# Performance work log

Measured on AMD Instinct MI355X. Metric: run time of the kernel, lower is better.

The kernel has to match this reference:

```python
import jax, jax.numpy as jnp
import numpy as np

N = 100000
E = 1600000
D_DES = 768
D = 128
NUM_REL = 2
SLOPE = 0.01  # torch LeakyReLU default negative slope


def leaky_relu(x):
    return jnp.where(x >= 0, x, SLOPE * x)


def setup_inputs() -> dict:
    key = jax.random.key(0)
    ks = jax.random.split(key, 16)
    s = 0.02
    return {
        "des": jax.random.normal(ks[0], (N, D_DES), jnp.float32),
        "tweet": jax.random.normal(ks[1], (N, D_DES), jnp.float32),
        "num_prop": jax.random.normal(ks[2], (N, 6), jnp.float32),
        "cat_prop": jax.random.normal(ks[3], (N, 11), jnp.float32),
        "edge_index": jax.random.randint(ks[4], (2, E), 0, N, jnp.int32),
        "edge_type": jax.random.randint(ks[5], (E,), 0, NUM_REL, jnp.int32),
        "W_des": s * jax.random.normal(ks[6], (D_DES, D), jnp.float32),
        "b_des": jnp.zeros((D,), jnp.float32),
        "W_in": s * jax.random.normal(ks[7], (D, D), jnp.float32),
        "b_in": jnp.zeros((D,), jnp.float32),
        "W_rel": s * jax.random.normal(ks[8], (NUM_REL, D, D), jnp.float32),
        "W_root": s * jax.random.normal(ks[9], (D, D), jnp.float32),
        "b_rgcn": jnp.zeros((D,), jnp.float32),
        "W_out1": s * jax.random.normal(ks[10], (D, D), jnp.float32),
        "b_out1": jnp.zeros((D,), jnp.float32),
        "W_out2": s * jax.random.normal(ks[11], (D, 2), jnp.float32),
        "b_out2": jnp.zeros((2,), jnp.float32),
    }


def rgcn_conv(x, src, dst, edge_type, W_rel, W_root, b):
    # PyG RGCNConv: out[i] = x[i] @ W_root + b + sum_r mean_{j in N_r(i)} x[j] @ W_r
    n = x.shape[0]
    out = x @ W_root + b
    for r in range(NUM_REL):
        mask = (edge_type == r).astype(x.dtype)  # [E]
        h = x @ W_rel[r]                         # [N, D] transform once per relation
        msg = h[src] * mask[:, None]             # [E, D] gather + mask
        agg = jax.ops.segment_sum(msg, dst, num_segments=n)   # [N, D]
        deg = jax.ops.segment_sum(mask, dst, num_segments=n)  # [N]
        out = out + agg / jnp.maximum(deg, 1.0)[:, None]
    return out


def reference(des, tweet, num_prop, cat_prop, edge_index, edge_type,
              W_des, b_des, W_in, b_in, W_rel, W_root, b_rgcn,
              W_out1, b_out1, W_out2, b_out2):
    src, dst = edge_index[0], edge_index[1]
    x = leaky_relu(des @ W_des + b_des)          # linear_relu_des (tweet/props unused in source)
    x = leaky_relu(x @ W_in + b_in)              # linear_relu_input
    x = rgcn_conv(x, src, dst, edge_type, W_rel, W_root, b_rgcn)
    # F.dropout with training=False is identity (eval mode)
    x = rgcn_conv(x, src, dst, edge_type, W_rel, W_root, b_rgcn)
    x = leaky_relu(x @ W_out1 + b_out1)          # linear_relu_output1
    x = x @ W_out2 + b_out2                      # linear_output2 -> [N, 2]
    return x
```

## Files before the change

kernel.cpp:

```cpp
#include <hip/hip_runtime.h>

#define SLOPE 0.01f

__device__ __forceinline__ float lrelu(float v) { return v >= 0.f ? v : SLOPE * v; }

template <int RELU>
__global__ __launch_bounds__(256, 2) void gemm128(const float* __restrict__ A,
                                                  const float* __restrict__ W,
                                                  const float* __restrict__ bias,
                                                  float* __restrict__ C,
                                                  int M, int K) {
    __shared__ float As[32][132];
    __shared__ float Ws[32][132];

    const int tid = threadIdx.x;
    const int m0 = blockIdx.x * 128;
    const int rg = tid >> 4;
    const int cg = tid & 15;
    const int lm = tid >> 3;
    const int lc = (tid & 7) * 4;
    const int wr = tid >> 5;
    const int wc = (tid & 31) * 4;

    float acc[8][8];
#pragma unroll
    for (int i = 0; i < 8; i++)
#pragma unroll
        for (int j = 0; j < 8; j++) acc[i][j] = 0.f;

    for (int k0 = 0; k0 < K; k0 += 32) {
#pragma unroll
        for (int p = 0; p < 4; p++) {
            int row = m0 + lm + p * 32;
            int rc = row < M ? row : M - 1;
            const float4 v = *(const float4*)(A + (size_t)rc * K + k0 + lc);
            As[lc + 0][lm + p * 32] = v.x;
            As[lc + 1][lm + p * 32] = v.y;
            As[lc + 2][lm + p * 32] = v.z;
            As[lc + 3][lm + p * 32] = v.w;
        }
#pragma unroll
        for (int p = 0; p < 4; p++) {
            *(float4*)&Ws[wr + p * 8][wc] =
                *(const float4*)(W + (size_t)(k0 + wr + p * 8) * 128 + wc);
        }
        __syncthreads();
#pragma unroll
        for (int kk = 0; kk < 32; kk++) {
            float a[8], b[8];
            *(float4*)&a[0] = *(const float4*)&As[kk][rg * 4];
            *(float4*)&a[4] = *(const float4*)&As[kk][64 + rg * 4];
            *(float4*)&b[0] = *(const float4*)&Ws[kk][cg * 4];
            *(float4*)&b[4] = *(const float4*)&Ws[kk][64 + cg * 4];
#pragma unroll
            for (int i = 0; i < 8; i++)
#pragma unroll
                for (int j = 0; j < 8; j++) acc[i][j] = fmaf(a[i], b[j], acc[i][j]);
        }
        __syncthreads();
    }

    float4 b0 = *(const float4*)(bias + cg * 4);
    float4 b1 = *(const float4*)(bias + 64 + cg * 4);
#pragma unroll
    for (int i = 0; i < 8; i++) {
        int row = m0 + ((i < 4) ? (rg * 4 + i) : (64 + rg * 4 + (i - 4)));
        if (row >= M) continue;
        float4 o0, o1;
        o0.x = acc[i][0] + b0.x; o0.y = acc[i][1] + b0.y;
        o0.z = acc[i][2] + b0.z; o0.w = acc[i][3] + b0.w;
        o1.x = acc[i][4] + b1.x; o1.y = acc[i][5] + b1.y;
        o1.z = acc[i][6] + b1.z; o1.w = acc[i][7] + b1.w;
        if (RELU) {
            o0.x = lrelu(o0.x); o0.y = lrelu(o0.y); o0.z = lrelu(o0.z); o0.w = lrelu(o0.w);
            o1.x = lrelu(o1.x); o1.y = lrelu(o1.y); o1.z = lrelu(o1.z); o1.w = lrelu(o1.w);
        }
        *(float4*)(C + (size_t)row * 128 + cg * 4) = o0;
        *(float4*)(C + (size_t)row * 128 + 64 + cg * 4) = o1;
    }
}

__global__ __launch_bounds__(256, 2) void rgcn_gemm(const float* __restrict__ x,
                                                    const float* __restrict__ agg0,
                                                    const float* __restrict__ agg1,
                                                    const float* __restrict__ Wroot,
                                                    const float* __restrict__ W0,
                                                    const float* __restrict__ W1,
                                                    const float* __restrict__ bias,
                                                    float* __restrict__ C, int M) {
    __shared__ float As[32][132];
    __shared__ float Ws[32][132];

    const int tid = threadIdx.x;
    const int m0 = blockIdx.x * 128;
    const int rg = tid >> 4;
    const int cg = tid & 15;
    const int lm = tid >> 3;
    const int lc = (tid & 7) * 4;
    const int wr = tid >> 5;
    const int wc = (tid & 31) * 4;

    float acc[8][8];
#pragma unroll
    for (int i = 0; i < 8; i++)
#pragma unroll
        for (int j = 0; j < 8; j++) acc[i][j] = 0.f;

    const float* Aseg[3] = {x, agg0, agg1};
    const float* Wseg[3] = {Wroot, W0, W1};

    for (int seg = 0; seg < 3; seg++) {
        const float* Ap = Aseg[seg];
        const float* Wp = Wseg[seg];
        for (int k0 = 0; k0 < 128; k0 += 32) {
#pragma unroll
            for (int p = 0; p < 4; p++) {
                int row = m0 + lm + p * 32;
                int rc = row < M ? row : M - 1;
                const float4 v = *(const float4*)(Ap + (size_t)rc * 128 + k0 + lc);
                As[lc + 0][lm + p * 32] = v.x;
                As[lc + 1][lm + p * 32] = v.y;
                As[lc + 2][lm + p * 32] = v.z;
                As[lc + 3][lm + p * 32] = v.w;
            }
#pragma unroll
            for (int p = 0; p < 4; p++) {
                *(float4*)&Ws[wr + p * 8][wc] =
                    *(const float4*)(Wp + (size_t)(k0 + wr + p * 8) * 128 + wc);
            }
            __syncthreads();
#pragma unroll
            for (int kk = 0; kk < 32; kk++) {
                float a[8], b[8];
                *(float4*)&a[0] = *(const float4*)&As[kk][rg * 4];
                *(float4*)&a[4] = *(const float4*)&As[kk][64 + rg * 4];
                *(float4*)&b[0] = *(const float4*)&Ws[kk][cg * 4];
                *(float4*)&b[4] = *(const float4*)&Ws[kk][64 + cg * 4];
#pragma unroll
                for (int i = 0; i < 8; i++)
#pragma unroll
                    for (int j = 0; j < 8; j++) acc[i][j] = fmaf(a[i], b[j], acc[i][j]);
            }
            __syncthreads();
        }
    }

    float4 b0 = *(const float4*)(bias + cg * 4);
    float4 b1 = *(const float4*)(bias + 64 + cg * 4);
#pragma unroll
    for (int i = 0; i < 8; i++) {
        int row = m0 + ((i < 4) ? (rg * 4 + i) : (64 + rg * 4 + (i - 4)));
        if (row >= M) continue;
        float4 o0, o1;
        o0.x = acc[i][0] + b0.x; o0.y = acc[i][1] + b0.y;
        o0.z = acc[i][2] + b0.z; o0.w = acc[i][3] + b0.w;
        o1.x = acc[i][4] + b1.x; o1.y = acc[i][5] + b1.y;
        o1.z = acc[i][6] + b1.z; o1.w = acc[i][7] + b1.w;
        *(float4*)(C + (size_t)row * 128 + cg * 4) = o0;
        *(float4*)(C + (size_t)row * 128 + 64 + cg * 4) = o1;
    }
}

__global__ __launch_bounds__(256) void hist_kernel(const int* __restrict__ ei,
                                                   const int* __restrict__ et,
                                                   int* __restrict__ cnt, int E, int N) {
    int e = blockIdx.x * 256 + threadIdx.x;
    if (e >= E) return;
    int d = ei[E + e];
    int r = et[e];
    atomicAdd(&cnt[r * N + d], 1);
}

__global__ __launch_bounds__(256) void scan_partial(const int* __restrict__ cnt,
                                                    int* __restrict__ partials, int n) {
    __shared__ int sm[256];
    int base = blockIdx.x * 1024;
    int t = threadIdx.x;
    int s = 0;
#pragma unroll
    for (int i = 0; i < 4; i++) {
        int idx = base + t * 4 + i;
        if (idx < n) s += cnt[idx];
    }
    sm[t] = s;
    __syncthreads();
    for (int off = 128; off; off >>= 1) {
        if (t < off) sm[t] += sm[t + off];
        __syncthreads();
    }
    if (t == 0) partials[blockIdx.x] = sm[0];
}

__global__ __launch_bounds__(64) void scan_top(int* __restrict__ partials, int nb,
                                               int* __restrict__ off, int n, int total) {
    int lane = threadIdx.x;
    int base = 0;
    for (int start = 0; start < nb; start += 64) {
        int idx = start + lane;
        int v = (idx < nb) ? partials[idx] : 0;
        int incl = v;
#pragma unroll
        for (int o = 1; o < 64; o <<= 1) {
            int t = __shfl_up(incl, o);
            if (lane >= o) incl += t;
        }
        if (idx < nb) partials[idx] = base + incl - v;
        base += __shfl(incl, 63);
    }
    if (lane == 0) off[n] = total;
}

__global__ __launch_bounds__(64) void scan_chunk(const int* __restrict__ cnt,
                                                 const int* __restrict__ partials,
                                                 int* __restrict__ off, int n) {
    int lane = threadIdx.x;
    int base = partials[blockIdx.x];
    int cbase = blockIdx.x * 1024;
    for (int i = 0; i < 16; i++) {
        int idx = cbase + i * 64 + lane;
        int v = (idx < n) ? cnt[idx] : 0;
        int incl = v;
#pragma unroll
        for (int o = 1; o < 64; o <<= 1) {
            int t = __shfl_up(incl, o);
            if (lane >= o) incl += t;
        }
        if (idx < n) off[idx] = base + incl - v;
        base += __shfl(incl, 63);
    }
}

__global__ __launch_bounds__(256) void scatter_kernel(const int* __restrict__ ei,
                                                      const int* __restrict__ et,
                                                      const int* __restrict__ off,
                                                      int* __restrict__ cur,
                                                      int* __restrict__ sorted_src,
                                                      int E, int N) {
    int e = blockIdx.x * 256 + threadIdx.x;
    if (e >= E) return;
    int s = ei[e];
    int d = ei[E + e];
    int r = et[e];
    int b = r * N + d;
    int pos = off[b] + atomicAdd(&cur[b], 1);
    sorted_src[pos] = s;
}

__global__ __launch_bounds__(256) void agg_csr(const int* __restrict__ off,
                                               const int* __restrict__ sorted_src,
                                               const float* __restrict__ X,
                                               float* __restrict__ agg0,
                                               float* __restrict__ agg1,
                                               int N) {
    int w = (int)((blockIdx.x * (unsigned)blockDim.x + threadIdx.x) >> 6);
    if (w >= 2 * N) return;
    int lane = threadIdx.x & 63;
    int start = off[w];
    int end = off[w + 1];
    float2 sum = {0.f, 0.f};
    for (int i = start; i < end; i++) {
        int s = sorted_src[i];
        float2 v = *(const float2*)(X + (size_t)s * 128 + lane * 2);
        sum.x += v.x;
        sum.y += v.y;
    }
    int deg = end - start;
    float inv = (deg > 1) ? (1.f / (float)deg) : 1.f;
    sum.x *= inv;
    sum.y *= inv;
    float* agg = (w < N) ? agg0 : agg1;
    int d = (w < N) ? w : w - N;
    *(float2*)(agg + (size_t)d * 128 + lane * 2) = sum;
}

__global__ __launch_bounds__(256) void out2_kernel(const float* __restrict__ X,
                                                   const float* __restrict__ W,
                                                   const float* __restrict__ b,
                                                   float* __restrict__ out, int M) {
    const int row = (int)((blockIdx.x * (unsigned)blockDim.x + threadIdx.x) >> 6);
    if (row >= M) return;
    const int lane = threadIdx.x & 63;
    const float* xr = X + (size_t)row * 128;
    float x0 = xr[lane], x1 = xr[lane + 64];
    float s0 = x0 * W[lane * 2 + 0] + x1 * W[(lane + 64) * 2 + 0];
    float s1 = x0 * W[lane * 2 + 1] + x1 * W[(lane + 64) * 2 + 1];
#pragma unroll
    for (int off = 32; off; off >>= 1) {
        s0 += __shfl_down(s0, off);
        s1 += __shfl_down(s1, off);
    }
    if (lane == 0) {
        out[(size_t)row * 2 + 0] = s0 + b[0];
        out[(size_t)row * 2 + 1] = s1 + b[1];
    }
}

extern "C" void kernel_launch(void* const* d_in, const int* in_sizes, int n_in,
                              void* d_out, int out_size, void* d_ws, size_t ws_size,
                              hipStream_t stream) {
    const float* des    = (const float*)d_in[0];
    const int*   ei     = (const int*)d_in[4];
    const int*   et     = (const int*)d_in[5];
    const float* W_des  = (const float*)d_in[6];
    const float* b_des  = (const float*)d_in[7];
    const float* W_in   = (const float*)d_in[8];
    const float* b_in   = (const float*)d_in[9];
    const float* W_rel  = (const float*)d_in[10];
    const float* W_root = (const float*)d_in[11];
    const float* b_rgcn = (const float*)d_in[12];
    const float* W_out1 = (const float*)d_in[13];
    const float* b_out1 = (const float*)d_in[14];
    const float* W_out2 = (const float*)d_in[15];
    const float* b_out2 = (const float*)d_in[16];
    float* out = (float*)d_out;

    const int N = in_sizes[0] / 768;
    const int E = in_sizes[5];
    const int TWO_N = 2 * N;
    const float* W0 = W_rel;
    const float* W1 = W_rel + 128 * 128;

    float* ws    = (float*)d_ws;
    float* xA    = ws;
    float* xB    = xA + (size_t)N * 128;
    float* agg0  = xB + (size_t)N * 128;
    float* agg1  = agg0 + (size_t)N * 128;
    int*   cnt   = (int*)(agg1 + (size_t)N * 128);
    int*   cur   = cnt + TWO_N;
    int*   off   = cur + TWO_N;
    int*   parts = off + TWO_N + 1;
    int*   ssrc  = parts + 256;

    const int gemmBlocks = (N + 127) / 128;
    const int edgeBlocks = (E + 255) / 256;
    const int aggBlocks  = (TWO_N + 3) / 4;
    const int rowBlocks  = (int)(((size_t)N * 64 + 255) / 256);
    const int nChunks    = (TWO_N + 1023) / 1024;

    hipMemsetAsync(cnt, 0, (size_t)2 * TWO_N * sizeof(int), stream);
    hist_kernel<<<edgeBlocks, 256, 0, stream>>>(ei, et, cnt, E, N);
    scan_partial<<<nChunks, 256, 0, stream>>>(cnt, parts, TWO_N);
    scan_top<<<1, 64, 0, stream>>>(parts, nChunks, off, TWO_N, E);
    scan_chunk<<<nChunks, 64, 0, stream>>>(cnt, parts, off, TWO_N);
    scatter_kernel<<<edgeBlocks, 256, 0, stream>>>(ei, et, off, cur, ssrc, E, N);

    gemm128<1><<<gemmBlocks, 256, 0, stream>>>(des, W_des, b_des, xA, N, 768);
    gemm128<1><<<gemmBlocks, 256, 0, stream>>>(xA, W_in, b_in, xB, N, 128);

    agg_csr<<<aggBlocks, 256, 0, stream>>>(off, ssrc, xB, agg0, agg1, N);
    rgcn_gemm<<<gemmBlocks, 256, 0, stream>>>(xB, agg0, agg1, W_root, W0, W1, b_rgcn, xA, N);

    agg_csr<<<aggBlocks, 256, 0, stream>>>(off, ssrc, xA, agg0, agg1, N);
    rgcn_gemm<<<gemmBlocks, 256, 0, stream>>>(xA, agg0, agg1, W_root, W0, W1, b_rgcn, xB, N);

    gemm128<1><<<gemmBlocks, 256, 0, stream>>>(xB, W_out1, b_out1, xA, N, 128);
    out2_kernel<<<rowBlocks, 256, 0, stream>>>(xA, W_out2, b_out2, out, N);
}
```

Measured before the change: 1.667 ms.

## Replace FP32 FMA GEMMs with split-bf16 MFMA GEMMs

```diff
diff --git a/kernel.cpp b/kernel.cpp
--- a/kernel.cpp
+++ b/kernel.cpp
@@ -2,162 +2,152 @@
 
 #define SLOPE 0.01f
 
+typedef __attribute__((ext_vector_type(8))) short bf16x8;
+typedef __attribute__((ext_vector_type(4))) float f32x4;
+
 __device__ __forceinline__ float lrelu(float v) { return v >= 0.f ? v : SLOPE * v; }
 
-template <int RELU>
-__global__ __launch_bounds__(256, 2) void gemm128(const float* __restrict__ A,
-                                                  const float* __restrict__ W,
-                                                  const float* __restrict__ bias,
-                                                  float* __restrict__ C,
-                                                  int M, int K) {
-    __shared__ float As[32][132];
-    __shared__ float Ws[32][132];
+__device__ __forceinline__ void split_bf16(float x, unsigned short& h, unsigned short& l) {
+    unsigned b = __float_as_uint(x);
+    unsigned hb = b & 0xFFFF0000u;
+    h = (unsigned short)(hb >> 16);
+    float r = x - __uint_as_float(hb);
+    l = (unsigned short)(__float_as_uint(r) >> 16);
+}
+
+__global__ __launch_bounds__(256) void split_w(const float* __restrict__ W_des,
+                                               const float* __restrict__ W_in,
+                                               const float* __restrict__ W_root,
+                                               const float* __restrict__ W0,
+                                               const float* __restrict__ W1,
+                                               const float* __restrict__ W_out1,
+                                               unsigned short* __restrict__ th,
+                                               unsigned short* __restrict__ tl) {
+    const float* src;
+    int K;
+    size_t off;
+    switch (blockIdx.y) {
+        case 0: src = W_des;  K = 768; off = 0;                    break;
+        case 1: src = W_in;   K = 128; off = 768 * 128;            break;
+        case 2: src = W_root; K = 128; off = 768 * 128 + 16384;    break;
+        case 3: src = W0;     K = 128; off = 768 * 128 + 2 * 16384; break;
+        case 4: src = W1;     K = 128; off = 768 * 128 + 3 * 16384; break;
+        default: src = W_out1; K = 128; off = 768 * 128 + 4 * 16384; break;
+    }
+    const int c = blockIdx.x;
+    unsigned short* dh = th + off + (size_t)c * K;
+    unsigned short* dl = tl + off + (size_t)c * K;
+    for (int k = threadIdx.x; k < K; k += 256) {
+        float v = src[(size_t)k * 128 + c];
+        unsigned short h, l;
+        split_bf16(v, h, l);
+        dh[k] = h;
+        dl[k] = l;
+    }
+}
+
+template <int NSEG, int RELU>
+__global__ __launch_bounds__(256, 2) void gemm_mfma(
+        const float* __restrict__ A0, const float* __restrict__ A1,
+        const float* __restrict__ A2,
+        const unsigned short* __restrict__ Wh0, const unsigned short* __restrict__ Wl0,
+        const unsigned short* __restrict__ Wh1, const unsigned short* __restrict__ Wl1,
+        const unsigned short* __restrict__ Wh2, const unsigned short* __restrict__ Wl2,
+        int K0, const float* __restrict__ bias, float* __restrict__ C, int M) {
+    __shared__ unsigned short AsH[128][32];
+    __shared__ unsigned short AsL[128][32];
+    __shared__ unsigned short BsH[128][32];
+    __shared__ unsigned short BsL[128][32];
 
     const int tid = threadIdx.x;
+    const int lane = tid & 63;
+    const int wv = tid >> 6;
+    const int wr = (wv >> 1) * 64;
+    const int wc = (wv & 1) * 64;
+    const int fr = lane & 15;
+    const int fk = (lane >> 4) * 8;
     const int m0 = blockIdx.x * 128;
-    const int rg = tid >> 4;
-    const int cg = tid & 15;
-    const int lm = tid >> 3;
-    const int lc = (tid & 7) * 4;
-    const int wr = tid >> 5;
-    const int wc = (tid & 31) * 4;
-
-    float acc[8][8];
-#pragma unroll
-    for (int i = 0; i < 8; i++)
-#pragma unroll
-        for (int j = 0; j < 8; j++) acc[i][j] = 0.f;
-
-    for (int k0 = 0; k0 < K; k0 += 32) {
-#pragma unroll
-        for (int p = 0; p < 4; p++) {
-            int row = m0 + lm + p * 32;
-            int rc = row < M ? row : M - 1;
-            const float4 v = *(const float4*)(A + (size_t)rc * K + k0 + lc);
-            As[lc + 0][lm + p * 32] = v.x;
-            As[lc + 1][lm + p * 32] = v.y;
-            As[lc + 2][lm + p * 32] = v.z;
-            As[lc + 3][lm + p * 32] = v.w;
-        }
-#pragma unroll
-        for (int p = 0; p < 4; p++) {
-            *(float4*)&Ws[wr + p * 8][wc] =
-                *(const float4*)(W + (size_t)(k0 + wr + p * 8) * 128 + wc);
-        }
-        __syncthreads();
-#pragma unroll
-        for (int kk = 0; kk < 32; kk++) {
-            float a[8], b[8];
-            *(float4*)&a[0] = *(const float4*)&As[kk][rg * 4];
-            *(float4*)&a[4] = *(const float4*)&As[kk][64 + rg * 4];
-            *(float4*)&b[0] = *(const float4*)&Ws[kk][cg * 4];
-            *(float4*)&b[4] = *(const float4*)&Ws[kk][64 + cg * 4];
-#pragma unroll
-            for (int i = 0; i < 8; i++)
-#pragma unroll
-                for (int j = 0; j < 8; j++) acc[i][j] = fmaf(a[i], b[j], acc[i][j]);
-        }
-        __syncthreads();
-    }
-
-    float4 b0 = *(const float4*)(bias + cg * 4);
-    float4 b1 = *(const float4*)(bias + 64 + cg * 4);
-#pragma unroll
-    for (int i = 0; i < 8; i++) {
-        int row = m0 + ((i < 4) ? (rg * 4 + i) : (64 + rg * 4 + (i - 4)));
-        if (row >= M) continue;
-        float4 o0, o1;
-        o0.x = acc[i][0] + b0.x; o0.y = acc[i][1] + b0.y;
-        o0.z = acc[i][2] + b0.z; o0.w = acc[i][3] + b0.w;
-        o1.x = acc[i][4] + b1.x; o1.y = acc[i][5] + b1.y;
-        o1.z = acc[i][6] + b1.z; o1.w = acc[i][7] + b1.w;
-        if (RELU) {
-            o0.x = lrelu(o0.x); o0.y = lrelu(o0.y); o0.z = lrelu(o0.z); o0.w = lrelu(o0.w);
-            o1.x = lrelu(o1.x); o1.y = lrelu(o1.y); o1.z = lrelu(o1.z); o1.w = lrelu(o1.w);
-        }
-        *(float4*)(C + (size_t)row * 128 + cg * 4) = o0;
-        *(float4*)(C + (size_t)row * 128 + 64 + cg * 4) = o1;
-    }
-}
-
-__global__ __launch_bounds__(256, 2) void rgcn_gemm(const float* __restrict__ x,
-                                                    const float* __restrict__ agg0,
-                                                    const float* __restrict__ agg1,
-                                                    const float* __restrict__ Wroot,
-                                                    const float* __restrict__ W0,
-                                                    const float* __restrict__ W1,
-                                                    const float* __restrict__ bias,
-                                                    float* __restrict__ C, int M) {
-    __shared__ float As[32][132];
-    __shared__ float Ws[32][132];
-
-    const int tid = threadIdx.x;
-    const int m0 = blockIdx.x * 128;
-    const int rg = tid >> 4;
-    const int cg = tid & 15;
-    const int lm = tid >> 3;
-    const int lc = (tid & 7) * 4;
-    const int wr = tid >> 5;
-    const int wc = (tid & 31) * 4;
-
-    float acc[8][8];
-#pragma unroll
-    for (int i = 0; i < 8; i++)
-#pragma unroll
-        for (int j = 0; j < 8; j++) acc[i][j] = 0.f;
-
-    const float* Aseg[3] = {x, agg0, agg1};
-    const float* Wseg[3] = {Wroot, W0, W1};
-
-    for (int seg = 0; seg < 3; seg++) {
-        const float* Ap = Aseg[seg];
-        const float* Wp = Wseg[seg];
-        for (int k0 = 0; k0 < 128; k0 += 32) {
-#pragma unroll
-            for (int p = 0; p < 4; p++) {
-                int row = m0 + lm + p * 32;
-                int rc = row < M ? row : M - 1;
-                const float4 v = *(const float4*)(Ap + (size_t)rc * 128 + k0 + lc);
-                As[lc + 0][lm + p * 32] = v.x;
-                As[lc + 1][lm + p * 32] = v.y;
-                As[lc + 2][lm + p * 32] = v.z;
-                As[lc + 3][lm + p * 32] = v.w;
-            }
-#pragma unroll
-            for (int p = 0; p < 4; p++) {
-                *(float4*)&Ws[wr + p * 8][wc] =
-                    *(const float4*)(Wp + (size_t)(k0 + wr + p * 8) * 128 + wc);
+
+    f32x4 acc[4][4];
+#pragma unroll
+    for (int i = 0; i < 4; ++i)
+#pragma unroll
+        for (int j = 0; j < 4; ++j)
+#pragma unroll
+            for (int r = 0; r < 4; ++r) acc[i][j][r] = 0.f;
+
+    for (int seg = 0; seg < NSEG; ++seg) {
+        const float* A = (seg == 0) ? A0 : (seg == 1 ? A1 : A2);
+        const unsigned short* Wh = (seg == 0) ? Wh0 : (seg == 1 ? Wh1 : Wh2);
+        const unsigned short* Wl = (seg == 0) ? Wl0 : (seg == 1 ? Wl1 : Wl2);
+        const int K = (seg == 0) ? K0 : 128;
+
+        for (int k0 = 0; k0 < K; k0 += 32) {
+#pragma unroll
+            for (int p = 0; p < 4; ++p) {
+                const int f = tid + 256 * p;
+                const int r = f >> 3;
+                const int q = f & 7;
+                int row = m0 + r;
+                if (row >= M) row = M - 1;
+                const float4 v = *(const float4*)(A + (size_t)row * K + k0 + q * 4);
+                unsigned short h0, h1, h2, h3, l0, l1, l2, l3;
+                split_bf16(v.x, h0, l0);
+                split_bf16(v.y, h1, l1);
+                split_bf16(v.z, h2, l2);
+                split_bf16(v.w, h3, l3);
+                *(ushort4*)&AsH[r][q * 4] = make_ushort4(h0, h1, h2, h3);
+                *(ushort4*)&AsL[r][q * 4] = make_ushort4(l0, l1, l2, l3);
+            }
+#pragma unroll
+            for (int p = 0; p < 4; ++p) {
+                const int f = tid + 256 * p;
+                const int c = f >> 3;
+                const int q = f & 7;
+                *(ushort4*)&BsH[c][q * 4] = *(const ushort4*)(Wh + (size_t)c * K + k0 + q * 4);
+                *(ushort4*)&BsL[c][q * 4] = *(const ushort4*)(Wl + (size_t)c * K + k0 + q * 4);
             }
             __syncthreads();
-#pragma unroll
-            for (int kk = 0; kk < 32; kk++) {
-                float a[8], b[8];
-                *(float4*)&a[0] = *(const float4*)&As[kk][rg * 4];
-                *(float4*)&a[4] = *(const float4*)&As[kk][64 + rg * 4];
-                *(float4*)&b[0] = *(const float4*)&Ws[kk][cg * 4];
-                *(float4*)&b[4] = *(const float4*)&Ws[kk][64 + cg * 4];
-#pragma unroll
-                for (int i = 0; i < 8; i++)
-#pragma unroll
-                    for (int j = 0; j < 8; j++) acc[i][j] = fmaf(a[i], b[j], acc[i][j]);
+
+            bf16x8 ah[4], al[4];
+#pragma unroll
+            for (int i = 0; i < 4; ++i) {
+                ah[i] = *(const bf16x8*)&AsH[wr + i * 16 + fr][fk];
+                al[i] = *(const bf16x8*)&AsL[wr + i * 16 + fr][fk];
+            }
+#pragma unroll
+            for (int j = 0; j < 4; ++j) {
+                const bf16x8 bh = *(const bf16x8*)&BsH[wc + j * 16 + fr][fk];
+                const bf16x8 bl = *(const bf16x8*)&BsL[wc + j * 16 + fr][fk];
+#pragma unroll
+                for (int i = 0; i < 4; ++i) {
+                    acc[i][j] = __builtin_amdgcn_mfma_f32_16x16x32_bf16(ah[i], bh, acc[i][j], 0, 0, 0);
+                    acc[i][j] = __builtin_amdgcn_mfma_f32_16x16x32_bf16(ah[i], bl, acc[i][j], 0, 0, 0);
+                    acc[i][j] = __builtin_amdgcn_mfma_f32_16x16x32_bf16(al[i], bh, acc[i][j], 0, 0, 0);
+                }
             }
             __syncthreads();
         }
     }
 
-    float4 b0 = *(const float4*)(bias + cg * 4);
-    float4 b1 = *(const float4*)(bias + 64 + cg * 4);
-#pragma unroll
-    for (int i = 0; i < 8; i++) {
-        int row = m0 + ((i < 4) ? (rg * 4 + i) : (64 + rg * 4 + (i - 4)));
-        if (row >= M) continue;
-        float4 o0, o1;
-        o0.x = acc[i][0] + b0.x; o0.y = acc[i][1] + b0.y;
-        o0.z = acc[i][2] + b0.z; o0.w = acc[i][3] + b0.w;
-        o1.x = acc[i][4] + b1.x; o1.y = acc[i][5] + b1.y;
-        o1.z = acc[i][6] + b1.z; o1.w = acc[i][7] + b1.w;
-        *(float4*)(C + (size_t)row * 128 + cg * 4) = o0;
-        *(float4*)(C + (size_t)row * 128 + 64 + cg * 4) = o1;
+    const int lr = (lane >> 4) * 4;
+    float bv[4];
+#pragma unroll
+    for (int j = 0; j < 4; ++j) bv[j] = bias[wc + j * 16 + fr];
+#pragma unroll
+    for (int i = 0; i < 4; ++i) {
+#pragma unroll
+        for (int r = 0; r < 4; ++r) {
+            const int row = m0 + wr + i * 16 + lr + r;
+            if (row >= M) continue;
+            float* cp = C + (size_t)row * 128 + wc;
+#pragma unroll
+            for (int j = 0; j < 4; ++j) {
+                float v = acc[i][j][r] + bv[j];
+                if (RELU) v = lrelu(v);
+                cp[j * 16 + fr] = v;
+            }
+        }
     }
 }
 
@@ -331,11 +321,24 @@
     int*   parts = off + TWO_N + 1;
     int*   ssrc  = parts + 256;
 
+    const size_t OFF_DES  = 0;
+    const size_t OFF_IN   = 768 * 128;
+    const size_t OFF_ROOT = OFF_IN + 16384;
+    const size_t OFF_W0   = OFF_ROOT + 16384;
+    const size_t OFF_W1   = OFF_W0 + 16384;
+    const size_t OFF_OUT1 = OFF_W1 + 16384;
+    const size_t WT_ELEMS = OFF_OUT1 + 16384;
+    uintptr_t wtbase = ((uintptr_t)(ssrc + E) + 15) & ~(uintptr_t)15;
+    unsigned short* wth = (unsigned short*)wtbase;
+    unsigned short* wtl = wth + WT_ELEMS;
+
     const int gemmBlocks = (N + 127) / 128;
     const int edgeBlocks = (E + 255) / 256;
     const int aggBlocks  = (TWO_N + 3) / 4;
     const int rowBlocks  = (int)(((size_t)N * 64 + 255) / 256);
     const int nChunks    = (TWO_N + 1023) / 1024;
+
+    split_w<<<dim3(128, 6, 1), 256, 0, stream>>>(W_des, W_in, W_root, W0, W1, W_out1, wth, wtl);
 
     hipMemsetAsync(cnt, 0, (size_t)2 * TWO_N * sizeof(int), stream);
     hist_kernel<<<edgeBlocks, 256, 0, stream>>>(ei, et, cnt, E, N);
@@ -344,15 +347,30 @@
     scan_chunk<<<nChunks, 64, 0, stream>>>(cnt, parts, off, TWO_N);
     scatter_kernel<<<edgeBlocks, 256, 0, stream>>>(ei, et, off, cur, ssrc, E, N);
 
-    gemm128<1><<<gemmBlocks, 256, 0, stream>>>(des, W_des, b_des, xA, N, 768);
-    gemm128<1><<<gemmBlocks, 256, 0, stream>>>(xA, W_in, b_in, xB, N, 128);
+    gemm_mfma<1, 1><<<gemmBlocks, 256, 0, stream>>>(
+        des, nullptr, nullptr,
+        wth + OFF_DES, wtl + OFF_DES, nullptr, nullptr, nullptr, nullptr,
+        768, b_des, xA, N);
+    gemm_mfma<1, 1><<<gemmBlocks, 256, 0, stream>>>(
+        xA, nullptr, nullptr,
+        wth + OFF_IN, wtl + OFF_IN, nullptr, nullptr, nullptr, nullptr,
+        128, b_in, xB, N);
 
     agg_csr<<<aggBlocks, 256, 0, stream>>>(off, ssrc, xB, agg0, agg1, N);
-    rgcn_gemm<<<gemmBlocks, 256, 0, stream>>>(xB, agg0, agg1, W_root, W0, W1, b_rgcn, xA, N);
+    gemm_mfma<3, 0><<<gemmBlocks, 256, 0, stream>>>(
+        xB, agg0, agg1,
+        wth + OFF_ROOT, wtl + OFF_ROOT, wth + OFF_W0, wtl + OFF_W0, wth + OFF_W1, wtl + OFF_W1,
+        128, b_rgcn, xA, N);
 
     agg_csr<<<aggBlocks, 256, 0, stream>>>(off, ssrc, xA, agg0, agg1, N);
-    rgcn_gemm<<<gemmBlocks, 256, 0, stream>>>(xA, agg0, agg1, W_root, W0, W1, b_rgcn, xB, N);
-
-    gemm128<1><<<gemmBlocks, 256, 0, stream>>>(xB, W_out1, b_out1, xA, N, 128);
+    gemm_mfma<3, 0><<<gemmBlocks, 256, 0, stream>>>(
+        xA, agg0, agg1,
+        wth + OFF_ROOT, wtl + OFF_ROOT, wth + OFF_W0, wtl + OFF_W0, wth + OFF_W1, wtl + OFF_W1,
+        128, b_rgcn, xB, N);
+
+    gemm_mfma<1, 1><<<gemmBlocks, 256, 0, stream>>>(
+        xB, nullptr, nullptr,
+        wth + OFF_OUT1, wtl + OFF_OUT1, nullptr, nullptr, nullptr, nullptr,
+        128, b_out1, xA, N);
     out2_kernel<<<rowBlocks, 256, 0, stream>>>(xA, W_out2, b_out2, out, N);
 }
```

Measured after the change: 1.440 ms. 1.16x faster.
